# Optimization experiments

Measured on AMD Instinct MI355X. Metric: run time of the kernel, lower is better.

Reference implementation:

```python
import jax, jax.numpy as jnp
import numpy as np

E, R, D, DFF, L, H, B, S = 10000, 200, 64, 256, 2, 8, 8, 1024
N = B * S            # total quadruples
QPQ = 3              # qualifiers per quadruple
Q = N * QPQ


def setup_inputs() -> dict:
    key = jax.random.key(0)
    ks = jax.random.split(key, 32)
    def nrm(k, shape, scale=0.05):
        return jax.random.normal(k, shape, dtype=jnp.float32) * scale
    return {
        # int index arrays (pre-tokenized entity/relation names)
        'head_idx': jax.random.randint(ks[0], (N,), 0, E, dtype=jnp.int32),
        'rel_idx': jax.random.randint(ks[1], (N,), 0, R, dtype=jnp.int32),
        'tail_idx': jax.random.randint(ks[2], (N,), 0, E, dtype=jnp.int32),
        'qual_type_idx': jax.random.randint(ks[3], (Q,), 0, R, dtype=jnp.int32),
        'qual_value_idx': jax.random.randint(ks[4], (Q,), 0, E, dtype=jnp.int32),
        'qual_seg': jnp.repeat(jnp.arange(N, dtype=jnp.int32), QPQ),  # sorted, every quad has >=1 qualifier
        # tokenizer params
        'entity_emb': nrm(ks[5], (E, D)),
        'rel_emb': nrm(ks[6], (R, D)),
        'mlp_W1': nrm(ks[7], (2 * D, D)),
        'mlp_b1': jnp.zeros((D,), jnp.float32),
        'mlp_W2': nrm(ks[8], (D, D)),
        'mlp_b2': jnp.zeros((D,), jnp.float32),
        'attn_w': nrm(ks[9], (D,)),  # AttentionAggregator scoring vector
        'proj_W': nrm(ks[10], (4 * D, D)),
        'proj_b': jnp.zeros((D,), jnp.float32),
        # transformer encoder params (post-norm, relu FFN), stacked over L layers
        'Wqkv': nrm(ks[11], (L, D, 3 * D)),
        'bqkv': jnp.zeros((L, 3 * D), jnp.float32),
        'Wo': nrm(ks[12], (L, D, D)),
        'bo': jnp.zeros((L, D), jnp.float32),
        'ln1_s': jnp.ones((L, D), jnp.float32),
        'ln1_b': jnp.zeros((L, D), jnp.float32),
        'Wff1': nrm(ks[13], (L, D, DFF)),
        'bff1': jnp.zeros((L, DFF), jnp.float32),
        'Wff2': nrm(ks[14], (L, DFF, D)),
        'bff2': jnp.zeros((L, D), jnp.float32),
        'ln2_s': jnp.ones((L, D), jnp.float32),
        'ln2_b': jnp.zeros((L, D), jnp.float32),
    }


def _ln(x, s, b):
    m = x.mean(-1, keepdims=True)
    v = ((x - m) ** 2).mean(-1, keepdims=True)
    return (x - m) / jnp.sqrt(v + 1e-5) * s + b


def _forward(head_idx, rel_idx, tail_idx, qual_type_idx, qual_value_idx, qual_seg,
             entity_emb, rel_emb, mlp_W1, mlp_b1, mlp_W2, mlp_b2, attn_w,
             proj_W, proj_b, Wqkv, bqkv, Wo, bo, ln1_s, ln1_b,
             Wff1, bff1, Wff2, bff2, ln2_s, ln2_b):
    # ---- qualifier MLP over all qualifiers at once: [Q, 2D] -> [Q, D]
    qx = jnp.concatenate([rel_emb[qual_type_idx], entity_emb[qual_value_idx]], axis=-1)
    pq = jax.nn.relu(qx @ mlp_W1 + mlp_b1) @ mlp_W2 + mlp_b2  # [Q, D]
    # ---- ragged per-quadruple attention pooling as a segment softmax
    s = pq @ attn_w                                            # [Q]
    m = jax.ops.segment_max(s, qual_seg, num_segments=N)       # [N]
    e = jnp.exp(s - m[qual_seg])
    den = jax.ops.segment_sum(e, qual_seg, num_segments=N)
    w = e / den[qual_seg]
    agg = jax.ops.segment_sum(pq * w[:, None], qual_seg, num_segments=N)  # [N, D]
    # ---- token assembly: gather + concat + linear projection
    tok_in = jnp.concatenate(
        [entity_emb[head_idx], rel_emb[rel_idx], entity_emb[tail_idx], agg], axis=-1)  # [N, 4D]
    x = (tok_in @ proj_W + proj_b).reshape(B, S, D)
    # ---- transformer encoder (post-norm, relu, no dropout)
    dh = D // H
    scale = 1.0 / np.sqrt(dh).astype(np.float32)
    for i in range(L):
        qkv = x @ Wqkv[i] + bqkv[i]
        q, k, v = jnp.split(qkv, 3, axis=-1)
        q = q.reshape(B, S, H, dh)
        k = k.reshape(B, S, H, dh)
        v = v.reshape(B, S, H, dh)
        att = jax.nn.softmax(jnp.einsum('bqhd,bkhd->bhqk', q, k) * scale, axis=-1)
        o = jnp.einsum('bhqk,bkhd->bqhd', att, v).reshape(B, S, D) @ Wo[i] + bo[i]
        x = _ln(x + o, ln1_s[i], ln1_b[i])
        f = jax.nn.relu(x @ Wff1[i] + bff1[i]) @ Wff2[i] + bff2[i]
        x = _ln(x + f, ln2_s[i], ln2_b[i])
    return x  # [B, S, D]


def reference(head_idx, rel_idx, tail_idx, qual_type_idx, qual_value_idx, qual_seg,
              entity_emb, rel_emb, mlp_W1, mlp_b1, mlp_W2, mlp_b2, attn_w,
              proj_W, proj_b, Wqkv, bqkv, Wo, bo, ln1_s, ln1_b,
              Wff1, bff1, Wff2, bff2, ln2_s, ln2_b):
    return _forward(head_idx, rel_idx, tail_idx, qual_type_idx, qual_value_idx, qual_seg,
                    entity_emb, rel_emb, mlp_W1, mlp_b1, mlp_W2, mlp_b2, attn_w,
                    proj_W, proj_b, Wqkv, bqkv, Wo, bo, ln1_s, ln1_b,
                    Wff1, bff1, Wff2, bff2, ln2_s, ln2_b)
```

## Files before the change

kernel.cpp:

```cpp
#include <hip/hip_runtime.h>
#include <hip/hip_bf16.h>
#include <hip/hip_fp16.h>

constexpr int E = 10000, R = 200, D = 64, DFF = 256, L = 2, H = 8, B = 8, S = 1024;
constexpr int N = B * S;
constexpr int QPQ = 3;
constexpr int QQ = N * QPQ;
constexpr int DH = D / H;

typedef _Float16 h2 __attribute__((ext_vector_type(2)));
typedef __fp16 fp16x2 __attribute__((ext_vector_type(2)));
typedef _Float16 f16x4 __attribute__((ext_vector_type(4)));
typedef _Float16 f16x8 __attribute__((ext_vector_type(8)));
typedef float f32x4 __attribute__((ext_vector_type(4)));
union F4H { float4 f4; h2 h[4]; f16x8 v8; };

__device__ __forceinline__ h2 pack2(float a, float b) {
#if __has_builtin(__builtin_amdgcn_cvt_pkrtz)
    fp16x2 r = __builtin_amdgcn_cvt_pkrtz(a, b);
    return __builtin_bit_cast(h2, r);
#else
    h2 r; r.x = (_Float16)a; r.y = (_Float16)b; return r;
#endif
}
__device__ __forceinline__ f32x4 mfma16(f16x8 a, f16x8 b, f32x4 c) {
    return __builtin_amdgcn_mfma_f32_16x16x32_f16(a, b, c, 0, 0, 0);
}
__device__ __forceinline__ f32x4 mfma16k16(f16x4 a, f16x4 b, f32x4 c) {
    return __builtin_amdgcn_mfma_f32_16x16x16f16(a, b, c, 0, 0, 0);
}

__device__ __forceinline__ float wsum64(float v) {
#pragma unroll
    for (int off = 32; off; off >>= 1) v += __shfl_xor(v, off, 64);
    return v;
}

constexpr int OFFB_WO   = 0;
constexpr int OFFB_WF1  = 4096;
constexpr int OFFB_WF2  = 20480;
constexpr int OFFB_WQKV = 36864;
constexpr int BFRAG_PER_LAYER = 49152;
constexpr int BF_THREADS = 12288;

constexpr int OFFB2_W1   = 0;
constexpr int OFFB2_W2   = 8192;
constexpr int OFFB2_PROJ = 12288;
constexpr int BF2_THREADS = 3584;
constexpr int PREP_THREADS = BF_THREADS + BF2_THREADS;

__global__ void prep_all(const float* __restrict__ Wo, const float* __restrict__ Wf1,
                         const float* __restrict__ Wf2, const float* __restrict__ Wqkv,
                         const float* __restrict__ W1, const float* __restrict__ W2,
                         const float* __restrict__ projW,
                         _Float16* __restrict__ out, _Float16* __restrict__ out2) {
    const int t0 = blockIdx.x * 256 + threadIdx.x;
    if (t0 < BF_THREADS) {
        const int t = t0;
        const int l = t / 6144;
        int u = t - l * 6144;
        const int lane = u & 63;
        const int ar = lane & 15, ag = lane >> 4;
        const float* src; int Nn, t_n, s, off, chunk;
        if (u < 512) {
            chunk = u >> 6; t_n = chunk >> 1; s = chunk & 1;
            src = Wo + l * 4096; Nn = 64; off = OFFB_WO;
        } else if (u < 2560) { u -= 512;
            chunk = u >> 6; t_n = chunk >> 1; s = chunk & 1;
            src = Wf1 + l * 16384; Nn = 256; off = OFFB_WF1;
        } else if (u < 4608) { u -= 2560;
            chunk = u >> 6; t_n = chunk >> 3; s = chunk & 7;
            src = Wf2 + l * 16384; Nn = 64; off = OFFB_WF2;
        } else { u -= 4608;
            chunk = u >> 6; t_n = chunk >> 1; s = chunk & 1;
            src = Wqkv + l * 12288; Nn = 192; off = OFFB_WQKV;
        }
        _Float16* dst = out + (size_t)l * BFRAG_PER_LAYER + off + ((size_t)chunk * 64 + lane) * 8;
        const int col = t_n * 16 + ar;
#pragma unroll
        for (int i = 0; i < 8; i++) {
            const int k = s * 32 + ag * 8 + i;
            dst[i] = (_Float16)src[k * Nn + col];
        }
        return;
    }
    const int t = t0 - BF_THREADS;
    if (t >= BF2_THREADS) return;
    const int lane = t & 63;
    const int ar = lane & 15, ag = lane >> 4;
    const float* src; int t_n, s, off, chunk;
    if (t < 1024) {
        chunk = t >> 6; t_n = chunk >> 2; s = chunk & 3;
        src = W1; off = OFFB2_W1;
    } else if (t < 1536) {
        const int u = t - 1024;
        chunk = u >> 6; t_n = chunk >> 1; s = chunk & 1;
        src = W2; off = OFFB2_W2;
    } else {
        const int u = t - 1536;
        chunk = u >> 6; t_n = chunk >> 3; s = chunk & 7;
        src = projW; off = OFFB2_PROJ;
    }
    _Float16* dst = out2 + off + ((size_t)chunk * 64 + lane) * 8;
    const int col = t_n * 16 + ar;
#pragma unroll
    for (int i = 0; i < 8; i++) {
        const int k = s * 32 + ag * 8 + i;
        dst[i] = (_Float16)src[k * 64 + col];
    }
}

__global__ __launch_bounds__(256, 2)
void front_kernel(const int* __restrict__ head, const int* __restrict__ rel,
                  const int* __restrict__ tail,
                  const int* __restrict__ qt, const int* __restrict__ qv,
                  const float* __restrict__ ent_emb, const float* __restrict__ rel_emb,
                  const _Float16* __restrict__ W1B, const float* __restrict__ b1,
                  const _Float16* __restrict__ W2B, const float* __restrict__ b2,
                  const float* __restrict__ attn_w,
                  const _Float16* __restrict__ projB, const float* __restrict__ projb,
                  const _Float16* __restrict__ qkv0B, const float* __restrict__ bqkv0,
                  float* __restrict__ x, _Float16* __restrict__ qkvh) {
    const int tid = threadIdx.x, wave = tid >> 6, lane = tid & 63;
    const int n0 = blockIdx.x * 16;
    const int q0 = n0 * 3;
    const int ar = lane & 15, ag = lane >> 4;

    __shared__ _Float16 qx[48][136];
    __shared__ _Float16 hs[48][72];
    __shared__ _Float16 ps[48][72];
    __shared__ _Float16 tok[16][264];
    __shared__ _Float16 act[16][72];
    __shared__ int qts[48], qvs[48], hd[16], rl[16], tl[16];
    __shared__ float s_lds[48];
    __shared__ float wsf[16][3];

    if (tid < 48) qts[tid] = qt[q0 + tid];
    else if (tid < 96) qvs[tid - 48] = qv[q0 + tid - 48];
    else if (tid < 112) hd[tid - 96] = head[n0 + tid - 96];
    else if (tid < 128) rl[tid - 112] = rel[n0 + tid - 112];
    else if (tid < 144) tl[tid - 128] = tail[n0 + tid - 128];

    f16x8 w1f[4];
#pragma unroll
    for (int s = 0; s < 4; s++)
        w1f[s] = *(const f16x8*)&W1B[((size_t)(wave * 4 + s) * 64 + lane) * 8];
    const int colw = wave * 16 + ar;
    const float bb1 = b1[colw], bb2 = b2[colw];
    __syncthreads();

#pragma unroll
    for (int i = 0; i < 24; i++) {
        const int f = tid + i * 256;
        const int row = f >> 7, col = f & 127;
        const float v = (col < 64) ? rel_emb[qts[row] * D + col]
                                   : ent_emb[(size_t)qvs[row] * D + (col - 64)];
        qx[row][col] = (_Float16)v;
    }
    f16x8 w2f[2];
#pragma unroll
    for (int s = 0; s < 2; s++)
        w2f[s] = *(const f16x8*)&W2B[((size_t)(wave * 2 + s) * 64 + lane) * 8];
    __syncthreads();

    {
#pragma unroll
        for (int rt = 0; rt < 3; rt++) {
            f32x4 c = {0.f, 0.f, 0.f, 0.f};
#pragma unroll
            for (int s = 0; s < 4; s++) {
                const f16x8 a = *(const f16x8*)&qx[rt * 16 + ar][s * 32 + ag * 8];
                c = mfma16(a, w1f[s], c);
            }
#pragma unroll
            for (int j = 0; j < 4; j++)
                hs[rt * 16 + ag * 4 + j][colw] = (_Float16)fmaxf(c[j] + bb1, 0.f);
        }
    }
    f16x8 pjf[8];
#pragma unroll
    for (int st = 0; st < 8; st++)
        pjf[st] = *(const f16x8*)&projB[((size_t)(wave * 8 + st) * 64 + lane) * 8];
    __syncthreads();

    {
#pragma unroll
        for (int rt = 0; rt < 3; rt++) {
            f32x4 c = {0.f, 0.f, 0.f, 0.f};
#pragma unroll
            for (int s = 0; s < 2; s++) {
                const f16x8 a = *(const f16x8*)&hs[rt * 16 + ar][s * 32 + ag * 8];
                c = mfma16(a, w2f[s], c);
            }
#pragma unroll
            for (int j = 0; j < 4; j++)
                ps[rt * 16 + ag * 4 + j][colw] = (_Float16)(c[j] + bb2);
        }
    }
    __syncthreads();

    {
        const float aw = attn_w[lane];
#pragma unroll
        for (int r = 0; r < 12; r++) {
            const int row = wave * 12 + r;
            const float sv = wsum64((float)ps[row][lane] * aw);
            if (lane == 0) s_lds[row] = sv;
        }
    }
    __syncthreads();
    if (tid < 16) {
        const float s0 = s_lds[tid * 3 + 0], s1 = s_lds[tid * 3 + 1], s2 = s_lds[tid * 3 + 2];
        const float mm = fmaxf(s0, fmaxf(s1, s2));
        const float e0 = __expf(s0 - mm), e1 = __expf(s1 - mm), e2 = __expf(s2 - mm);
        const float rd = 1.f / (e0 + e1 + e2);
        wsf[tid][0] = e0 * rd; wsf[tid][1] = e1 * rd; wsf[tid][2] = e2 * rd;
    }
    __syncthreads();

#pragma unroll
    for (int i = 0; i < 16; i++) {
        const int f = tid + i * 256;
        const int row = f >> 8, col = f & 255;
        float v;
        if (col < 64)       v = ent_emb[(size_t)hd[row] * D + col];
        else if (col < 128) v = rel_emb[rl[row] * D + (col - 64)];
        else if (col < 192) v = ent_emb[(size_t)tl[row] * D + (col - 128)];
        else {
            const int c = col - 192;
            v = wsf[row][0] * (float)ps[row * 3 + 0][c] +
                wsf[row][1] * (float)ps[row * 3 + 1][c] +
                wsf[row][2] * (float)ps[row * 3 + 2][c];
        }
        tok[row][col] = (_Float16)v;
    }
    f16x8 qvf[6];
#pragma unroll
    for (int tt = 0; tt < 3; tt++) {
        const int tn = wave * 3 + tt;
        qvf[2 * tt]     = *(const f16x8*)&qkv0B[((size_t)(tn * 2 + 0) * 64 + lane) * 8];
        qvf[2 * tt + 1] = *(const f16x8*)&qkv0B[((size_t)(tn * 2 + 1) * 64 + lane) * 8];
    }
    __syncthreads();

    {
        f32x4 c = {0.f, 0.f, 0.f, 0.f};
#pragma unroll
        for (int st = 0; st < 8; st++) {
            const f16x8 a = *(const f16x8*)&tok[ar][st * 32 + ag * 8];
            c = mfma16(a, pjf[st], c);
        }
        const float bb = projb[colw];
#pragma unroll
        for (int j = 0; j < 4; j++) {
            const int row = ag * 4 + j;
            const float xv = c[j] + bb;
            x[(size_t)(n0 + row) * D + colw] = xv;
            act[row][colw] = (_Float16)xv;
        }
    }
    __syncthreads();

    {
        const f16x8 a0 = *(const f16x8*)&act[ar][ag * 8];
        const f16x8 a1 = *(const f16x8*)&act[ar][32 + ag * 8];
#pragma unroll
        for (int tt = 0; tt < 3; tt++) {
            const int tn = wave * 3 + tt;
            f32x4 c = {0.f, 0.f, 0.f, 0.f};
            c = mfma16(a0, qvf[2 * tt], c);
            c = mfma16(a1, qvf[2 * tt + 1], c);
            const int col = tn * 16 + ar;
            const float bb = bqkv0[col];
#pragma unroll
            for (int j = 0; j < 4; j++)
                qkvh[(size_t)(n0 + ag * 4 + j) * 192 + col] = (_Float16)(c[j] + bb);
        }
    }
}

__global__ __launch_bounds__(256, 4)
void attn_kernel(const _Float16* __restrict__ qkvh, _Float16* __restrict__ out) {
    const int bid = blockIdx.x;
    const int qc = bid & 15;
    const int h = (bid >> 4) & 7;
    const int b = bid >> 7;
    const int tid = threadIdx.x, wave = tid >> 6, lane = tid & 63;
    const int ar = lane & 15, ag = lane >> 4;

    constexpr int VP = 1032;
    __shared__ _Float16 Kl[S][8];
    __shared__ _Float16 Vt[8][VP];

    const _Float16* base = qkvh + (size_t)b * S * 192;

    const int q0 = qc * 64 + wave * 16;
    f16x4 qf = {};
    if (ag < 2)
        qf = *(const f16x4*)(base + (size_t)(q0 + ar) * 192 + h * 8 + ag * 4);

    const _Float16 sch = (_Float16)0.3535533905932738f;
    const h2 sc2 = {sch, sch};
    for (int it = 0; it < 4; it++) {
        const int key = it * 256 + tid;
        F4H u; u.f4 = *(const float4*)(base + (size_t)key * 192 + 64 + h * 8);
#pragma unroll
        for (int i = 0; i < 4; i++) u.h[i] = u.h[i] * sc2;
        *(float4*)&Kl[key][0] = u.f4;
        F4H v; v.f4 = *(const float4*)(base + (size_t)key * 192 + 128 + h * 8);
        const _Float16* vp = (const _Float16*)&v;
#pragma unroll
        for (int d = 0; d < 8; d++) Vt[d][key] = vp[d];
    }
    __syncthreads();

    f32x4 oacc0 = {0.f, 0.f, 0.f, 0.f}, oacc1 = {0.f, 0.f, 0.f, 0.f};
    float lsum0 = 0.f, lsum1 = 0.f;
    const int vd = ar & 7;
    for (int t = 0; t < 64; t += 2) {
#pragma unroll
        for (int uu = 0; uu < 2; uu++) {
            const int k16 = (t + uu) * 16;
            const f16x4 kf = *(const f16x4*)&Kl[k16 + ar][(ag & 1) * 4];
            f32x4 s4 = {0.f, 0.f, 0.f, 0.f};
            s4 = mfma16k16(kf, qf, s4);
            const float p0 = __expf(s4[0]), p1 = __expf(s4[1]);
            const float p2 = __expf(s4[2]), p3 = __expf(s4[3]);
            union { h2 q[2]; f16x4 v; } pu;
            pu.q[0] = pack2(p0, p1); pu.q[1] = pack2(p2, p3);
            const f16x4 vf = *(const f16x4*)&Vt[vd][k16 + ag * 4];
            if (uu == 0) {
                lsum0 += (p0 + p1) + (p2 + p3);
                oacc0 = mfma16k16(pu.v, vf, oacc0);
            } else {
                lsum1 += (p0 + p1) + (p2 + p3);
                oacc1 = mfma16k16(pu.v, vf, oacc1);
            }
        }
    }
    float lsum = lsum0 + lsum1;
    f32x4 oacc;
#pragma unroll
    for (int j = 0; j < 4; j++) oacc[j] = oacc0[j] + oacc1[j];
    lsum += __shfl_xor(lsum, 16, 64);
    lsum += __shfl_xor(lsum, 32, 64);
    _Float16* op = out + ((size_t)(b * S + q0)) * 64 + h * 8;
#pragma unroll
    for (int j = 0; j < 4; j++) {
        const float lq = __shfl(lsum, 4 * ag + j, 64);
        if (ar < 8)
            op[(size_t)(4 * ag + j) * 64 + ar] = (_Float16)(oacc[j] / lq);
    }
}

__global__ __launch_bounds__(256, 2)
void fused_tail_kernel(float* __restrict__ x, const _Float16* __restrict__ att16,
                       const _Float16* __restrict__ WoB, const float* __restrict__ bo,
                       const float* __restrict__ ln1s, const float* __restrict__ ln1b,
                       const _Float16* __restrict__ Wf1B, const float* __restrict__ bf1,
                       const _Float16* __restrict__ Wf2B, const float* __restrict__ bf2,
                       const float* __restrict__ ln2s, const float* __restrict__ ln2b,
                       const _Float16* __restrict__ WqB, const float* __restrict__ bqkvN,
                       _Float16* __restrict__ qkvh, int do_qkv) {
    const int tid = threadIdx.x, wave = tid >> 6, lane = tid & 63;
    const int n0 = blockIdx.x * 16;
    const int ar = lane & 15, ag = lane >> 4;
    const int colw = wave * 16 + ar;

    __shared__ float    xs0[16][76];
    __shared__ _Float16 xs1[16][72];
    __shared__ _Float16 f1s[16][264];

    {
        const f16x8 a0 = *(const f16x8*)&att16[((size_t)(n0 + ar)) * 64 + ag * 8];
        const f16x8 a1 = *(const f16x8*)&att16[((size_t)(n0 + ar)) * 64 + 32 + ag * 8];
        const f16x8 b0 = *(const f16x8*)&WoB[((size_t)(wave * 2 + 0) * 64 + lane) * 8];
        const f16x8 b1 = *(const f16x8*)&WoB[((size_t)(wave * 2 + 1) * 64 + lane) * 8];
        float res[4];
#pragma unroll
        for (int j = 0; j < 4; j++)
            res[j] = x[(size_t)(n0 + ag * 4 + j) * D + colw];
        f32x4 c = {0.f, 0.f, 0.f, 0.f};
        c = mfma16(a0, b0, c);
        c = mfma16(a1, b1, c);
        const float bb = bo[colw];
#pragma unroll
        for (int j = 0; j < 4; j++)
            xs0[ag * 4 + j][colw] = res[j] + c[j] + bb;
    }
    f16x8 w1f[8];
#pragma unroll
    for (int tt = 0; tt < 4; tt++) {
        const int tn = wave * 4 + tt;
        w1f[2 * tt]     = *(const f16x8*)&Wf1B[((size_t)(tn * 2 + 0) * 64 + lane) * 8];
        w1f[2 * tt + 1] = *(const f16x8*)&Wf1B[((size_t)(tn * 2 + 1) * 64 + lane) * 8];
    }
    __syncthreads();

    {
        const float l1s_ = ln1s[lane], l1b_ = ln1b[lane];
#pragma unroll
        for (int r = 0; r < 4; r++) {
            const int row = wave * 4 + r;
            const float t = xs0[row][lane];
            const float mean = wsum64(t) * (1.f / 64.f);
            const float dv = t - mean;
            const float var = wsum64(dv * dv) * (1.f / 64.f);
            xs1[row][lane] = (_Float16)(dv * rsqrtf(var + 1e-5f) * l1s_ + l1b_);
        }
    }
    f16x8 w2f[8];
#pragma unroll
    for (int s = 0; s < 8; s++)
        w2f[s] = *(const f16x8*)&Wf2B[((size_t)(wave * 8 + s) * 64 + lane) * 8];
    __syncthreads();

    {
        const f16x8 a0 = *(const f16x8*)&xs1[ar][ag * 8];
        const f16x8 a1 = *(const f16x8*)&xs1[ar][32 + ag * 8];
#pragma unroll
        for (int tt = 0; tt < 4; tt++) {
            const int tn = wave * 4 + tt;
            f32x4 c = {0.f, 0.f, 0.f, 0.f};
            c = mfma16(a0, w1f[2 * tt], c);
            c = mfma16(a1, w1f[2 * tt + 1], c);
            const int col = tn * 16 + ar;
            const float bb = bf1[col];
#pragma unroll
            for (int j = 0; j < 4; j++)
                f1s[ag * 4 + j][col] = (_Float16)fmaxf(c[j] + bb, 0.f);
        }
    }
    f16x8 qvf[6];
    if (do_qkv) {
#pragma unroll
        for (int tt = 0; tt < 3; tt++) {
            const int tn = wave * 3 + tt;
            qvf[2 * tt]     = *(const f16x8*)&WqB[((size_t)(tn * 2 + 0) * 64 + lane) * 8];
            qvf[2 * tt + 1] = *(const f16x8*)&WqB[((size_t)(tn * 2 + 1) * 64 + lane) * 8];
        }
    }
    __syncthreads();

    {
        f32x4 c = {0.f, 0.f, 0.f, 0.f};
#pragma unroll
        for (int s = 0; s < 8; s++) {
            const f16x8 a = *(const f16x8*)&f1s[ar][s * 32 + ag * 8];
            c = mfma16(a, w2f[s], c);
        }
        const float bb = bf2[colw];
#pragma unroll
        for (int j = 0; j < 4; j++) {
            const int row = ag * 4 + j;
            xs0[row][colw] = (float)xs1[row][colw] + c[j] + bb;
        }
    }
    __syncthreads();

    {
        const float l2s_ = ln2s[lane], l2b_ = ln2b[lane];
#pragma unroll
        for (int r = 0; r < 4; r++) {
            const int row = wave * 4 + r;
            const float t = xs0[row][lane];
            const float mean = wsum64(t) * (1.f / 64.f);
            const float dv = t - mean;
            const float var = wsum64(dv * dv) * (1.f / 64.f);
            const float xo = dv * rsqrtf(var + 1e-5f) * l2s_ + l2b_;
            x[(size_t)(n0 + row) * D + lane] = xo;
            xs1[row][lane] = (_Float16)xo;
        }
    }
    if (!do_qkv) return;
    __syncthreads();

    {
        const f16x8 a0 = *(const f16x8*)&xs1[ar][ag * 8];
        const f16x8 a1 = *(const f16x8*)&xs1[ar][32 + ag * 8];
#pragma unroll
        for (int tt = 0; tt < 3; tt++) {
            const int tn = wave * 3 + tt;
            f32x4 c = {0.f, 0.f, 0.f, 0.f};
            c = mfma16(a0, qvf[2 * tt], c);
            c = mfma16(a1, qvf[2 * tt + 1], c);
            const int col = tn * 16 + ar;
            const float bb = bqkvN[col];
#pragma unroll
            for (int j = 0; j < 4; j++)
                qkvh[(size_t)(n0 + ag * 4 + j) * 192 + col] = (_Float16)(c[j] + bb);
        }
    }
}

extern "C" void kernel_launch(void* const* d_in, const int* in_sizes, int n_in,
                              void* d_out, int out_size, void* d_ws, size_t ws_size,
                              hipStream_t stream) {
    const int*   head_idx  = (const int*)d_in[0];
    const int*   rel_idx   = (const int*)d_in[1];
    const int*   tail_idx  = (const int*)d_in[2];
    const int*   qual_type = (const int*)d_in[3];
    const int*   qual_val  = (const int*)d_in[4];
    const float* ent_emb = (const float*)d_in[6];
    const float* rel_emb = (const float*)d_in[7];
    const float* mlp_W1  = (const float*)d_in[8];
    const float* mlp_b1  = (const float*)d_in[9];
    const float* mlp_W2  = (const float*)d_in[10];
    const float* mlp_b2  = (const float*)d_in[11];
    const float* attn_w  = (const float*)d_in[12];
    const float* proj_W  = (const float*)d_in[13];
    const float* proj_b  = (const float*)d_in[14];
    const float* Wqkv    = (const float*)d_in[15];
    const float* bqkv    = (const float*)d_in[16];
    const float* Wo      = (const float*)d_in[17];
    const float* bo      = (const float*)d_in[18];
    const float* ln1_s   = (const float*)d_in[19];
    const float* ln1_b   = (const float*)d_in[20];
    const float* Wff1    = (const float*)d_in[21];
    const float* bff1    = (const float*)d_in[22];
    const float* Wff2    = (const float*)d_in[23];
    const float* bff2    = (const float*)d_in[24];
    const float* ln2_s   = (const float*)d_in[25];
    const float* ln2_b   = (const float*)d_in[26];

    float* x = (float*)d_out;

    _Float16* att16 = (_Float16*)d_ws;
    _Float16* qkvh  = att16 + (size_t)N * 64;
    _Float16* wbf   = qkvh + (size_t)N * 192;
    _Float16* wbf2  = wbf + (size_t)2 * BFRAG_PER_LAYER;

    prep_all<<<(PREP_THREADS + 255) / 256, 256, 0, stream>>>(
        Wo, Wff1, Wff2, Wqkv, mlp_W1, mlp_W2, proj_W, wbf, wbf2);
    front_kernel<<<N / 16, 256, 0, stream>>>(head_idx, rel_idx, tail_idx,
                                             qual_type, qual_val, ent_emb, rel_emb,
                                             wbf2 + OFFB2_W1, mlp_b1,
                                             wbf2 + OFFB2_W2, mlp_b2, attn_w,
                                             wbf2 + OFFB2_PROJ, proj_b,
                                             wbf + OFFB_WQKV, bqkv, x, qkvh);
    for (int l = 0; l < L; l++) {
        attn_kernel<<<B * H * (S / 64), 256, 0, stream>>>(qkvh, att16);
        const int nl = (l + 1 < L) ? (l + 1) : 0;
        const _Float16* wb = wbf + (size_t)l * BFRAG_PER_LAYER;
        fused_tail_kernel<<<N / 16, 256, 0, stream>>>(
            x, att16,
            wb + OFFB_WO, bo + l * D, ln1_s + l * D, ln1_b + l * D,
            wb + OFFB_WF1, bff1 + l * DFF,
            wb + OFFB_WF2, bff2 + l * D,
            ln2_s + l * D, ln2_b + l * D,
            wbf + (size_t)nl * BFRAG_PER_LAYER + OFFB_WQKV, bqkv + nl * 3 * D,
            qkvh, (l + 1 < L) ? 1 : 0);
    }
}
```

Baseline: 79.09 us.

## Run fused tail with one wave per 16-row block, removing block barriers

Changes fused_tail_kernel from four waves splitting output columns to a single 64-thread wave that computes all columns for its 16 rows. LayerNorm now reduces within 16-lane groups on register-held MFMA outputs, so the fp32 staging buffer and every __syncthreads go away. In exchange each wave issues four times as many MFMAs and weight loads, and register pressure rises from the larger per-thread accumulator arrays. LDS traffic between wave-local phases now relies on in-wave ordering alone.

```diff
diff --git a/kernel.cpp b/kernel.cpp
--- a/kernel.cpp
+++ b/kernel.cpp
@@ -33,6 +33,11 @@
 __device__ __forceinline__ float wsum64(float v) {
 #pragma unroll
     for (int off = 32; off; off >>= 1) v += __shfl_xor(v, off, 64);
+    return v;
+}
+__device__ __forceinline__ float sum16(float v) {
+#pragma unroll
+    for (int m = 1; m < 16; m <<= 1) v += __shfl_xor(v, m, 64);
     return v;
 }
 
@@ -353,7 +358,7 @@
     }
 }
 
-__global__ __launch_bounds__(256, 2)
+__global__ __launch_bounds__(64, 4)
 void fused_tail_kernel(float* __restrict__ x, const _Float16* __restrict__ att16,
                        const _Float16* __restrict__ WoB, const float* __restrict__ bo,
                        const float* __restrict__ ln1s, const float* __restrict__ ln1b,
@@ -362,129 +367,114 @@
                        const float* __restrict__ ln2s, const float* __restrict__ ln2b,
                        const _Float16* __restrict__ WqB, const float* __restrict__ bqkvN,
                        _Float16* __restrict__ qkvh, int do_qkv) {
-    const int tid = threadIdx.x, wave = tid >> 6, lane = tid & 63;
+    const int lane = threadIdx.x;
     const int n0 = blockIdx.x * 16;
     const int ar = lane & 15, ag = lane >> 4;
-    const int colw = wave * 16 + ar;
-
-    __shared__ float    xs0[16][76];
+
     __shared__ _Float16 xs1[16][72];
     __shared__ _Float16 f1s[16][264];
 
-    {
-        const f16x8 a0 = *(const f16x8*)&att16[((size_t)(n0 + ar)) * 64 + ag * 8];
-        const f16x8 a1 = *(const f16x8*)&att16[((size_t)(n0 + ar)) * 64 + 32 + ag * 8];
-        const f16x8 b0 = *(const f16x8*)&WoB[((size_t)(wave * 2 + 0) * 64 + lane) * 8];
-        const f16x8 b1 = *(const f16x8*)&WoB[((size_t)(wave * 2 + 1) * 64 + lane) * 8];
-        float res[4];
-#pragma unroll
-        for (int j = 0; j < 4; j++)
-            res[j] = x[(size_t)(n0 + ag * 4 + j) * D + colw];
+    const f16x8 a0 = *(const f16x8*)&att16[((size_t)(n0 + ar)) * 64 + ag * 8];
+    const f16x8 a1 = *(const f16x8*)&att16[((size_t)(n0 + ar)) * 64 + 32 + ag * 8];
+    float pre[4][4];
+#pragma unroll
+    for (int t = 0; t < 4; t++) {
+        const f16x8 b0 = *(const f16x8*)&WoB[((size_t)(t * 2 + 0) * 64 + lane) * 8];
+        const f16x8 b1 = *(const f16x8*)&WoB[((size_t)(t * 2 + 1) * 64 + lane) * 8];
         f32x4 c = {0.f, 0.f, 0.f, 0.f};
         c = mfma16(a0, b0, c);
         c = mfma16(a1, b1, c);
-        const float bb = bo[colw];
+        const int col = t * 16 + ar;
+        const float bb = bo[col];
 #pragma unroll
         for (int j = 0; j < 4; j++)
-            xs0[ag * 4 + j][colw] = res[j] + c[j] + bb;
-    }
-    f16x8 w1f[8];
-#pragma unroll
-    for (int tt = 0; tt < 4; tt++) {
-        const int tn = wave * 4 + tt;
-        w1f[2 * tt]     = *(const f16x8*)&Wf1B[((size_t)(tn * 2 + 0) * 64 + lane) * 8];
-        w1f[2 * tt + 1] = *(const f16x8*)&Wf1B[((size_t)(tn * 2 + 1) * 64 + lane) * 8];
-    }
-    __syncthreads();
-
-    {
-        const float l1s_ = ln1s[lane], l1b_ = ln1b[lane];
-#pragma unroll
-        for (int r = 0; r < 4; r++) {
-            const int row = wave * 4 + r;
-            const float t = xs0[row][lane];
-            const float mean = wsum64(t) * (1.f / 64.f);
-            const float dv = t - mean;
-            const float var = wsum64(dv * dv) * (1.f / 64.f);
-            xs1[row][lane] = (_Float16)(dv * rsqrtf(var + 1e-5f) * l1s_ + l1b_);
-        }
-    }
-    f16x8 w2f[8];
-#pragma unroll
-    for (int s = 0; s < 8; s++)
-        w2f[s] = *(const f16x8*)&Wf2B[((size_t)(wave * 8 + s) * 64 + lane) * 8];
-    __syncthreads();
-
-    {
-        const f16x8 a0 = *(const f16x8*)&xs1[ar][ag * 8];
-        const f16x8 a1 = *(const f16x8*)&xs1[ar][32 + ag * 8];
-#pragma unroll
-        for (int tt = 0; tt < 4; tt++) {
-            const int tn = wave * 4 + tt;
+            pre[t][j] = x[(size_t)(n0 + ag * 4 + j) * D + col] + c[j] + bb;
+    }
+    float l1sv[4], l1bv[4];
+#pragma unroll
+    for (int t = 0; t < 4; t++) { l1sv[t] = ln1s[t * 16 + ar]; l1bv[t] = ln1b[t * 16 + ar]; }
+    float xh[4][4];
+#pragma unroll
+    for (int j = 0; j < 4; j++) {
+        float s = (pre[0][j] + pre[1][j]) + (pre[2][j] + pre[3][j]);
+        const float mean = sum16(s) * (1.f / 64.f);
+        float v = 0.f;
+#pragma unroll
+        for (int t = 0; t < 4; t++) { const float d = pre[t][j] - mean; v += d * d; }
+        const float rs = rsqrtf(sum16(v) * (1.f / 64.f) + 1e-5f);
+#pragma unroll
+        for (int t = 0; t < 4; t++) {
+            xh[t][j] = (pre[t][j] - mean) * rs * l1sv[t] + l1bv[t];
+            xs1[ag * 4 + j][t * 16 + ar] = (_Float16)xh[t][j];
+        }
+    }
+    {
+        const f16x8 xa0 = *(const f16x8*)&xs1[ar][ag * 8];
+        const f16x8 xa1 = *(const f16x8*)&xs1[ar][32 + ag * 8];
+#pragma unroll
+        for (int tt = 0; tt < 16; tt++) {
+            const f16x8 b0 = *(const f16x8*)&Wf1B[((size_t)(tt * 2 + 0) * 64 + lane) * 8];
+            const f16x8 b1 = *(const f16x8*)&Wf1B[((size_t)(tt * 2 + 1) * 64 + lane) * 8];
             f32x4 c = {0.f, 0.f, 0.f, 0.f};
-            c = mfma16(a0, w1f[2 * tt], c);
-            c = mfma16(a1, w1f[2 * tt + 1], c);
-            const int col = tn * 16 + ar;
+            c = mfma16(xa0, b0, c);
+            c = mfma16(xa1, b1, c);
+            const int col = tt * 16 + ar;
             const float bb = bf1[col];
 #pragma unroll
             for (int j = 0; j < 4; j++)
                 f1s[ag * 4 + j][col] = (_Float16)fmaxf(c[j] + bb, 0.f);
         }
     }
-    f16x8 qvf[6];
-    if (do_qkv) {
-#pragma unroll
-        for (int tt = 0; tt < 3; tt++) {
-            const int tn = wave * 3 + tt;
-            qvf[2 * tt]     = *(const f16x8*)&WqB[((size_t)(tn * 2 + 0) * 64 + lane) * 8];
-            qvf[2 * tt + 1] = *(const f16x8*)&WqB[((size_t)(tn * 2 + 1) * 64 + lane) * 8];
-        }
-    }
-    __syncthreads();
-
-    {
-        f32x4 c = {0.f, 0.f, 0.f, 0.f};
-#pragma unroll
-        for (int s = 0; s < 8; s++) {
-            const f16x8 a = *(const f16x8*)&f1s[ar][s * 32 + ag * 8];
-            c = mfma16(a, w2f[s], c);
-        }
-        const float bb = bf2[colw];
-#pragma unroll
-        for (int j = 0; j < 4; j++) {
-            const int row = ag * 4 + j;
-            xs0[row][colw] = (float)xs1[row][colw] + c[j] + bb;
-        }
-    }
-    __syncthreads();
-
-    {
-        const float l2s_ = ln2s[lane], l2b_ = ln2b[lane];
-#pragma unroll
-        for (int r = 0; r < 4; r++) {
-            const int row = wave * 4 + r;
-            const float t = xs0[row][lane];
-            const float mean = wsum64(t) * (1.f / 64.f);
-            const float dv = t - mean;
-            const float var = wsum64(dv * dv) * (1.f / 64.f);
-            const float xo = dv * rsqrtf(var + 1e-5f) * l2s_ + l2b_;
-            x[(size_t)(n0 + row) * D + lane] = xo;
-            xs1[row][lane] = (_Float16)xo;
+    float pre2[4][4];
+    {
+        f16x8 fa[8];
+#pragma unroll
+        for (int s = 0; s < 8; s++) fa[s] = *(const f16x8*)&f1s[ar][s * 32 + ag * 8];
+#pragma unroll
+        for (int t = 0; t < 4; t++) {
+            f32x4 c = {0.f, 0.f, 0.f, 0.f};
+#pragma unroll
+            for (int s = 0; s < 8; s++) {
+                const f16x8 b = *(const f16x8*)&Wf2B[((size_t)(t * 8 + s) * 64 + lane) * 8];
+                c = mfma16(fa[s], b, c);
+            }
+            const int col = t * 16 + ar;
+            const float bb = bf2[col];
+#pragma unroll
+            for (int j = 0; j < 4; j++)
+                pre2[t][j] = xh[t][j] + c[j] + bb;
+        }
+    }
+    float l2sv[4], l2bv[4];
+#pragma unroll
+    for (int t = 0; t < 4; t++) { l2sv[t] = ln2s[t * 16 + ar]; l2bv[t] = ln2b[t * 16 + ar]; }
+#pragma unroll
+    for (int j = 0; j < 4; j++) {
+        float s = (pre2[0][j] + pre2[1][j]) + (pre2[2][j] + pre2[3][j]);
+        const float mean = sum16(s) * (1.f / 64.f);
+        float v = 0.f;
+#pragma unroll
+        for (int t = 0; t < 4; t++) { const float d = pre2[t][j] - mean; v += d * d; }
+        const float rs = rsqrtf(sum16(v) * (1.f / 64.f) + 1e-5f);
+#pragma unroll
+        for (int t = 0; t < 4; t++) {
+            const float xo = (pre2[t][j] - mean) * rs * l2sv[t] + l2bv[t];
+            x[(size_t)(n0 + ag * 4 + j) * D + t * 16 + ar] = xo;
+            xs1[ag * 4 + j][t * 16 + ar] = (_Float16)xo;
         }
     }
     if (!do_qkv) return;
-    __syncthreads();
-
-    {
-        const f16x8 a0 = *(const f16x8*)&xs1[ar][ag * 8];
-        const f16x8 a1 = *(const f16x8*)&xs1[ar][32 + ag * 8];
-#pragma unroll
-        for (int tt = 0; tt < 3; tt++) {
-            const int tn = wave * 3 + tt;
+    {
+        const f16x8 qa0 = *(const f16x8*)&xs1[ar][ag * 8];
+        const f16x8 qa1 = *(const f16x8*)&xs1[ar][32 + ag * 8];
+#pragma unroll
+        for (int tt = 0; tt < 12; tt++) {
+            const f16x8 b0 = *(const f16x8*)&WqB[((size_t)(tt * 2 + 0) * 64 + lane) * 8];
+            const f16x8 b1 = *(const f16x8*)&WqB[((size_t)(tt * 2 + 1) * 64 + lane) * 8];
             f32x4 c = {0.f, 0.f, 0.f, 0.f};
-            c = mfma16(a0, qvf[2 * tt], c);
-            c = mfma16(a1, qvf[2 * tt + 1], c);
-            const int col = tn * 16 + ar;
+            c = mfma16(qa0, b0, c);
+            c = mfma16(qa1, b1, c);
+            const int col = tt * 16 + ar;
             const float bb = bqkvN[col];
 #pragma unroll
             for (int j = 0; j < 4; j++)
@@ -542,7 +532,7 @@
         attn_kernel<<<B * H * (S / 64), 256, 0, stream>>>(qkvh, att16);
         const int nl = (l + 1 < L) ? (l + 1) : 0;
         const _Float16* wb = wbf + (size_t)l * BFRAG_PER_LAYER;
-        fused_tail_kernel<<<N / 16, 256, 0, stream>>>(
+        fused_tail_kernel<<<N / 16, 64, 0, stream>>>(
             x, att16,
             wb + OFFB_WO, bo + l * D, ln1_s + l * D, ln1_b + l * D,
             wb + OFFB_WF1, bff1 + l * DFF,
```

Result: slower. 81.00 us (+2.4%).
